# Optimization experiments

Measured on AMD Instinct MI355X. Metric: run time of the kernel, lower is better.

Reference implementation:

```python
import jax, jax.numpy as jnp
import numpy as np

N_LAYER, N_HEAD, N_EMBD, BLOCK, B, T = 8, 8, 1024, 1024, 2, 1024
LN_EPS = 1e-5


def _ln(x, w, b):
    m = jnp.mean(x, axis=-1, keepdims=True)
    v = jnp.mean(jnp.square(x - m), axis=-1, keepdims=True)
    return (x - m) * jax.lax.rsqrt(v + LN_EPS) * w + b


def setup_inputs() -> dict:
    key = jax.random.key(0)
    ks = jax.random.split(key, 8)
    L, C = N_LAYER, N_EMBD
    rn = lambda k, shape, s=0.02: jax.random.normal(k, shape, jnp.float32) * s
    return {
        "x": jax.random.normal(ks[0], (B, T, C), jnp.float32),
        "wpe": rn(ks[1], (BLOCK, C)),
        "ln1_w": jnp.ones((L, C), jnp.float32),
        "ln1_b": jnp.zeros((L, C), jnp.float32),
        "attn_w": rn(ks[2], (L, 3 * C, C)),
        "attn_b": jnp.zeros((L, 3 * C), jnp.float32),
        "proj_w": rn(ks[3], (L, C, C), 0.02 / np.sqrt(2 * L)),
        "proj_b": jnp.zeros((L, C), jnp.float32),
        "ln2_w": jnp.ones((L, C), jnp.float32),
        "ln2_b": jnp.zeros((L, C), jnp.float32),
        "fc_w": rn(ks[4], (L, 4 * C, C)),
        "fc_b": jnp.zeros((L, 4 * C), jnp.float32),
        "fcp_w": rn(ks[5], (L, C, 4 * C), 0.02 / np.sqrt(2 * L)),
        "fcp_b": jnp.zeros((L, C), jnp.float32),
        "lnf_w": jnp.ones((C,), jnp.float32),
        "lnf_b": jnp.zeros((C,), jnp.float32),
    }


def reference(x, wpe, ln1_w, ln1_b, attn_w, attn_b, proj_w, proj_b,
              ln2_w, ln2_b, fc_w, fc_b, fcp_w, fcp_b, lnf_w, lnf_b):
    Bb, Tt, C = x.shape
    H = N_HEAD
    D = C // H
    scale = jnp.float32(1.0 / np.sqrt(D))
    h = x + wpe[:Tt][None]  # pos emb broadcast over batch; dropout = identity (eval)
    causal = jnp.tril(jnp.ones((Tt, Tt), bool))  # [T,T]

    def block(h, p):
        l1w, l1b, aw, ab, pw, pb, l2w, l2b, fw, fb, pw2, pb2 = p
        xn = _ln(h, l1w, l1b)
        qkv = xn @ aw.T + ab  # [B,T,3C]
        q, k, v = jnp.split(qkv, 3, axis=-1)
        q = q.reshape(Bb, Tt, H, D).transpose(0, 2, 1, 3)  # bhtd
        k = k.reshape(Bb, Tt, H, D).transpose(0, 2, 1, 3)
        v = v.reshape(Bb, Tt, H, D).transpose(0, 2, 1, 3)
        att = jnp.einsum('bhtd,bhsd->bhts', q, k) * scale
        att = jnp.where(causal, att, -jnp.inf)
        att = jax.nn.softmax(att, axis=-1)
        y = jnp.einsum('bhts,bhsd->bhtd', att, v)
        y = y.transpose(0, 2, 1, 3).reshape(Bb, Tt, C)
        h = h + (y @ pw.T + pb)
        xn2 = _ln(h, l2w, l2b)
        m = jax.nn.gelu(xn2 @ fw.T + fb, approximate=True)  # matches NewGELU tanh form
        h = h + (m @ pw2.T + pb2)
        return h, None

    h, _ = jax.lax.scan(block, h, (ln1_w, ln1_b, attn_w, attn_b, proj_w, proj_b,
                                   ln2_w, ln2_b, fc_w, fc_b, fcp_w, fcp_b))
    return _ln(h, lnf_w, lnf_b)
```

## Files before the change

### kernel.cpp

```cpp
#include <hip/hip_runtime.h>

typedef unsigned short u16;
typedef __attribute__((ext_vector_type(8))) short short8;
typedef __attribute__((ext_vector_type(4))) float floatx4;

__device__ __forceinline__ u16 f2b(float f){
  unsigned u = __builtin_bit_cast(unsigned, f);
  u += 0x7FFFu + ((u >> 16) & 1u);
  return (u16)(u >> 16);
}

__device__ __forceinline__ float gelu_f(float x){
  float u = 0.7978845608028654f * (x + 0.044715f * x * x * x);
  float e = __expf(2.0f * u);
  return 0.5f * x * (2.0f - 2.0f / (e + 1.0f));
}

typedef const __attribute__((address_space(1))) unsigned int gas_u32;
typedef __attribute__((address_space(3))) unsigned int las_u32;
__device__ __forceinline__ void gll16(const void* g, void* l){
  __builtin_amdgcn_global_load_lds((gas_u32*)g, (las_u32*)l, 16, 0, 0);
}

__global__ __launch_bounds__(256) void k_cvt(const float* __restrict__ src,
                                             u16* __restrict__ dst){
  size_t e = ((size_t)blockIdx.x * 256 + threadIdx.x) * 4;
  float4 v = *(const float4*)(src + e);
  ushort4 o; o.x = f2b(v.x); o.y = f2b(v.y); o.z = f2b(v.z); o.w = f2b(v.w);
  *(ushort4*)(dst + e) = o;
}

__global__ __launch_bounds__(256) void k_addpos(const float* __restrict__ x,
                                                const float* __restrict__ wpe,
                                                float* __restrict__ h){
  size_t e = ((size_t)blockIdx.x * 256 + threadIdx.x) * 4;
  float4 a = *(const float4*)(x + e);
  float4 p = *(const float4*)(wpe + (e & 1048575u));
  float4 o; o.x = a.x + p.x; o.y = a.y + p.y; o.z = a.z + p.z; o.w = a.w + p.w;
  *(float4*)(h + e) = o;
}

__global__ __launch_bounds__(256) void k_layernorm(const float* __restrict__ x,
                                                   const float* __restrict__ w,
                                                   const float* __restrict__ b,
                                                   void* __restrict__ out, int out_bf16){
  int row = blockIdx.x, t = threadIdx.x;
  const float* xr = x + (size_t)row * 1024;
  float4 v = ((const float4*)xr)[t];
  float s1 = v.x + v.y + v.z + v.w;
  float s2 = v.x*v.x + v.y*v.y + v.z*v.z + v.w*v.w;
  #pragma unroll
  for (int off = 32; off > 0; off >>= 1){
    s1 += __shfl_down(s1, off);
    s2 += __shfl_down(s2, off);
  }
  __shared__ float p1[4], p2[4];
  if ((t & 63) == 0){ p1[t >> 6] = s1; p2[t >> 6] = s2; }
  __syncthreads();
  float S1 = p1[0] + p1[1] + p1[2] + p1[3];
  float S2 = p2[0] + p2[1] + p2[2] + p2[3];
  float mean = S1 * (1.0f / 1024.0f);
  float var  = S2 * (1.0f / 1024.0f) - mean * mean;
  float rs = rsqrtf(var + 1e-5f);
  float4 wv = ((const float4*)w)[t];
  float4 bv = ((const float4*)b)[t];
  float o0 = (v.x - mean) * rs * wv.x + bv.x;
  float o1 = (v.y - mean) * rs * wv.y + bv.y;
  float o2 = (v.z - mean) * rs * wv.z + bv.z;
  float o3 = (v.w - mean) * rs * wv.w + bv.w;
  if (out_bf16){
    ushort4 o; o.x = f2b(o0); o.y = f2b(o1); o.z = f2b(o2); o.w = f2b(o3);
    ((ushort4*)((u16*)out + (size_t)row * 1024))[t] = o;
  } else {
    float4 o; o.x = o0; o.y = o1; o.z = o2; o.w = o3;
    ((float4*)((float*)out + (size_t)row * 1024))[t] = o;
  }
}

template<int MODE>
__global__ __launch_bounds__(256) void k_gemm(
    const u16* __restrict__ A, int lda, long long A_bs, long long A_hs,
    const u16* __restrict__ B, int ldb, long long B_bs, long long B_hs,
    const float* __restrict__ bias,
    void* __restrict__ Out, int ldo, long long O_bs, long long O_hs,
    int Kdim, float scale, int causal, int n_ntiles, int Ksplit)
{
  int bx = blockIdx.x, by = blockIdx.y, bz = blockIdx.z;
  int nt = bx % n_ntiles, sp = bx / n_ntiles;
  if (MODE == 3 && nt > by) return;
  int m0 = by * 128, n0 = nt * 128;
  int kend_eff = (causal == 1) ? (m0 + 128 < Kdim ? m0 + 128 : Kdim) : Kdim;
  int ks = sp * Ksplit;
  int ke = ks + Ksplit < kend_eff ? ks + Ksplit : kend_eff;
  if (ks >= ke) return;
  int zb = bz >> 3, zh = bz & 7;
  A += (size_t)zb * A_bs + (size_t)zh * A_hs;
  B += (size_t)zb * B_bs + (size_t)zh * B_hs;
  size_t o_off = (size_t)zb * O_bs + (size_t)zh * O_hs;

  __shared__ u16 As[128 * 32];
  __shared__ u16 Bs[128 * 32];
  int t = threadIdx.x;
  int lane = t & 63, wid = t >> 6;
  int wm = (wid >> 1) * 64, wn = (wid & 1) * 64;
  int quad = lane >> 4, tm = lane & 15;
  int ar = t >> 2, ac = (t & 3) * 8;
  const u16* Ab = A + (size_t)(m0 + ar) * lda + ac;
  const u16* Bb = B + (size_t)(n0 + ar) * ldb + ac;
  u16* AsP0 = &As[t * 8];           u16* AsP1 = &As[2048 + t * 8];
  u16* BsP0 = &Bs[t * 8];           u16* BsP1 = &Bs[2048 + t * 8];
  const size_t a64 = (size_t)64 * lda, b64 = (size_t)64 * ldb;

  floatx4 acc[4][4] = {};
  for (int k0 = ks; k0 < ke; k0 += 32){
    __syncthreads();
    gll16(Ab + k0,        AsP0);
    gll16(Ab + a64 + k0,  AsP1);
    gll16(Bb + k0,        BsP0);
    gll16(Bb + b64 + k0,  BsP1);
    __syncthreads();
    short8 af[4], bf[4];
    #pragma unroll
    for (int i = 0; i < 4; i++)
      af[i] = *(const short8*)&As[(wm + i * 16 + tm) * 32 + quad * 8];
    #pragma unroll
    for (int j = 0; j < 4; j++)
      bf[j] = *(const short8*)&Bs[(wn + j * 16 + tm) * 32 + quad * 8];
    #pragma unroll
    for (int i = 0; i < 4; i++)
      #pragma unroll
      for (int j = 0; j < 4; j++)
        acc[i][j] = __builtin_amdgcn_mfma_f32_16x16x32_bf16(af[i], bf[j], acc[i][j], 0, 0, 0);
  }
  #pragma unroll
  for (int j = 0; j < 4; j++){
    int col = n0 + wn + j * 16 + tm;
    float bc = 0.0f;
    if ((MODE == 0 || MODE == 1) && bias) bc = bias[col];
    if (MODE == 2 && sp == 0 && bias) bc = bias[col];
    #pragma unroll
    for (int i = 0; i < 4; i++){
      int row0 = m0 + wm + i * 16 + quad * 4;
      #pragma unroll
      for (int r = 0; r < 4; r++){
        float v = acc[i][j][r] + bc;
        size_t idx = o_off + (size_t)(row0 + r) * ldo + col;
        if (MODE == 0)      ((u16*)Out)[idx] = f2b(v);
        else if (MODE == 1) ((u16*)Out)[idx] = f2b(gelu_f(v));
        else if (MODE == 3) ((float*)Out)[idx] = v * scale;
        else                atomicAdd((float*)Out + idx, v);
      }
    }
  }
}

__global__ __launch_bounds__(256) void k_transpose_v(const u16* __restrict__ vsrc,
                                                     u16* __restrict__ vt){
  __shared__ u16 tile[64][66];
  int bh = blockIdx.z, b = bh >> 3, hh = bh & 7;
  int d0 = blockIdx.x * 64, s0 = blockIdx.y * 64;
  const u16* src = vsrc + (size_t)b * 3145728 + hh * 128;
  int t = threadIdx.x;
  {
    int sr = t >> 4, c4 = (t & 15) * 4;
    #pragma unroll
    for (int p = 0; p < 4; p++){
      int s = sr + p * 16;
      ushort4 v = *(const ushort4*)(src + (size_t)(s0 + s) * 3072 + d0 + c4);
      tile[s][c4 + 0] = v.x; tile[s][c4 + 1] = v.y;
      tile[s][c4 + 2] = v.z; tile[s][c4 + 3] = v.w;
    }
  }
  __syncthreads();
  {
    int dr = t >> 4, s4 = (t & 15) * 4;
    #pragma unroll
    for (int p = 0; p < 4; p++){
      int d = dr + p * 16;
      ushort4 o;
      o.x = tile[s4 + 0][d]; o.y = tile[s4 + 1][d];
      o.z = tile[s4 + 2][d]; o.w = tile[s4 + 3][d];
      *(ushort4*)(vt + (size_t)bh * 131072 + (size_t)(d0 + d) * 1024 + s0 + s4) = o;
    }
  }
}

__global__ __launch_bounds__(256) void k_softmax(float* __restrict__ S){
  int bh = blockIdx.x >> 10, i = blockIdx.x & 1023;
  float* row = S + ((size_t)bh << 20) + ((size_t)i << 10);
  int t = threadIdx.x, j0 = t * 4;
  float4 v;
  if (j0 <= i) v = ((const float4*)row)[t];
  else { v.x = 0.0f; v.y = 0.0f; v.z = 0.0f; v.w = 0.0f; }
  float mx = -3.0e38f;
  if (j0 + 0 <= i) mx = fmaxf(mx, v.x);
  if (j0 + 1 <= i) mx = fmaxf(mx, v.y);
  if (j0 + 2 <= i) mx = fmaxf(mx, v.z);
  if (j0 + 3 <= i) mx = fmaxf(mx, v.w);
  #pragma unroll
  for (int off = 32; off > 0; off >>= 1) mx = fmaxf(mx, __shfl_down(mx, off));
  __shared__ float pm[4], ps[4];
  if ((t & 63) == 0) pm[t >> 6] = mx;
  __syncthreads();
  mx = fmaxf(fmaxf(pm[0], pm[1]), fmaxf(pm[2], pm[3]));
  float e0 = (j0 + 0 <= i) ? __expf(v.x - mx) : 0.0f;
  float e1 = (j0 + 1 <= i) ? __expf(v.y - mx) : 0.0f;
  float e2 = (j0 + 2 <= i) ? __expf(v.z - mx) : 0.0f;
  float e3 = (j0 + 3 <= i) ? __expf(v.w - mx) : 0.0f;
  float s = e0 + e1 + e2 + e3;
  #pragma unroll
  for (int off = 32; off > 0; off >>= 1) s += __shfl_down(s, off);
  if ((t & 63) == 0) ps[t >> 6] = s;
  __syncthreads();
  s = ps[0] + ps[1] + ps[2] + ps[3];
  float inv = 1.0f / s;
  ushort4 o; o.x = f2b(e0 * inv); o.y = f2b(e1 * inv);
  o.z = f2b(e2 * inv); o.w = f2b(e3 * inv);
  ((ushort4*)row)[t] = o;
}

extern "C" void kernel_launch(void* const* d_in, const int* in_sizes, int n_in,
                              void* d_out, int out_size, void* d_ws, size_t ws_size,
                              hipStream_t stream){
  const float* x     = (const float*)d_in[0];
  const float* wpe   = (const float*)d_in[1];
  const float* ln1w  = (const float*)d_in[2];
  const float* ln1b  = (const float*)d_in[3];
  const float* attnw = (const float*)d_in[4];
  const float* attnb = (const float*)d_in[5];
  const float* projw = (const float*)d_in[6];
  const float* projb = (const float*)d_in[7];
  const float* ln2w  = (const float*)d_in[8];
  const float* ln2b  = (const float*)d_in[9];
  const float* fcw   = (const float*)d_in[10];
  const float* fcb   = (const float*)d_in[11];
  const float* fcpw  = (const float*)d_in[12];
  const float* fcpb  = (const float*)d_in[13];
  const float* lnfw  = (const float*)d_in[14];
  const float* lnfb  = (const float*)d_in[15];

  char* ws = (char*)d_ws;
  float* h   = (float*)(ws);
  u16*   xn  = (u16*)(ws + 8388608);
  u16*   qkv = (u16*)(ws + 12582912);
  u16*   vt  = (u16*)(ws + 25165824);
  float* S   = (float*)(ws + 29360128);
  u16*   yb  = (u16*)(ws + 29360128);
  u16*   mlp = (u16*)(ws + 33554432);
  float* ybf = (float*)(ws + 96468992);
  u16*   wb  = (u16*)(ws + 104857600);

  k_addpos<<<2048, 256, 0, stream>>>(x, wpe, h);
  for (int l = 0; l < 8; l++){
    k_layernorm<<<2048, 256, 0, stream>>>(h, ln1w + l * 1024, ln1b + l * 1024, xn, 1);
    k_cvt<<<3072, 256, 0, stream>>>(attnw + (size_t)l * 3145728, wb);
    k_gemm<0><<<dim3(24, 16, 1), 256, 0, stream>>>(
        xn, 1024, 0, 0, wb, 1024, 0, 0, attnb + l * 3072,
        qkv, 3072, 0, 0, 1024, 1.0f, 0, 24, 1024);
    k_transpose_v<<<dim3(2, 16, 16), 256, 0, stream>>>(qkv + 2048, vt);
    k_gemm<3><<<dim3(8, 8, 16), 256, 0, stream>>>(
        qkv, 3072, 3145728LL, 128LL, qkv + 1024, 3072, 3145728LL, 128LL,
        nullptr, S, 1024, 8388608LL, 1048576LL, 128, 0.08838834764831845f, 2, 8, 128);
    k_softmax<<<16384, 256, 0, stream>>>(S);
    hipMemsetAsync(ybf, 0, 8388608, stream);
    k_gemm<4><<<dim3(4, 8, 16), 256, 0, stream>>>(
        (const u16*)S, 2048, 16777216LL, 2097152LL, vt, 1024, 1048576LL, 131072LL,
        nullptr, ybf, 1024, 1048576LL, 128LL, 1024, 1.0f, 1, 1, 256);
    k_cvt<<<2048, 256, 0, stream>>>(ybf, yb);
    k_cvt<<<1024, 256, 0, stream>>>(projw + (size_t)l * 1048576, wb);
    k_gemm<2><<<dim3(32, 16, 1), 256, 0, stream>>>(
        yb, 1024, 0, 0, wb, 1024, 0, 0, projb + l * 1024,
        h, 1024, 0, 0, 1024, 1.0f, 0, 8, 256);
    k_layernorm<<<2048, 256, 0, stream>>>(h, ln2w + l * 1024, ln2b + l * 1024, xn, 1);
    k_cvt<<<4096, 256, 0, stream>>>(fcw + (size_t)l * 4194304, wb);
    k_gemm<1><<<dim3(32, 16, 1), 256, 0, stream>>>(
        xn, 1024, 0, 0, wb, 1024, 0, 0, fcb + l * 4096,
        mlp, 4096, 0, 0, 1024, 1.0f, 0, 32, 1024);
    k_cvt<<<4096, 256, 0, stream>>>(fcpw + (size_t)l * 4194304, wb);
    k_gemm<2><<<dim3(32, 16, 1), 256, 0, stream>>>(
        mlp, 4096, 0, 0, wb, 4096, 0, 0, fcpb + l * 1024,
        h, 1024, 0, 0, 4096, 1.0f, 0, 8, 1024);
  }
  k_layernorm<<<2048, 256, 0, stream>>>(h, lnfw, lnfb, (float*)d_out, 0);
  (void)in_sizes; (void)n_in; (void)out_size; (void)ws_size;
}
```

Measured before the change: 2.240 ms.

## Fuse attention into flash kernel and pre-convert all layer weights once

Replaces the materialized score GEMM, separate softmax, split-K PV GEMM with atomics, memset and fp32-to-bf16 conversion with a single flash-attention kernel. It uses online softmax and a causal loop over 64-key tiles, writing bf16 outputs directly. This removes the large fp32 score matrix round trips through memory and several launches per layer. Weight conversion to bf16 is also hoisted out of the layer loop into four upfront launches, which needs more workspace. The flash kernel launches only 256 blocks with causally imbalanced work, so it may underutilize the GPU.

```diff
diff --git a/kernel.cpp b/kernel.cpp
--- a/kernel.cpp
+++ b/kernel.cpp
@@ -79,24 +79,18 @@
 
 template<int MODE>
 __global__ __launch_bounds__(256) void k_gemm(
-    const u16* __restrict__ A, int lda, long long A_bs, long long A_hs,
-    const u16* __restrict__ B, int ldb, long long B_bs, long long B_hs,
+    const u16* __restrict__ A, int lda,
+    const u16* __restrict__ B, int ldb,
     const float* __restrict__ bias,
-    void* __restrict__ Out, int ldo, long long O_bs, long long O_hs,
-    int Kdim, float scale, int causal, int n_ntiles, int Ksplit)
+    void* __restrict__ Out, int ldo,
+    int Kdim, int n_ntiles, int Ksplit)
 {
-  int bx = blockIdx.x, by = blockIdx.y, bz = blockIdx.z;
+  int bx = blockIdx.x, by = blockIdx.y;
   int nt = bx % n_ntiles, sp = bx / n_ntiles;
-  if (MODE == 3 && nt > by) return;
   int m0 = by * 128, n0 = nt * 128;
-  int kend_eff = (causal == 1) ? (m0 + 128 < Kdim ? m0 + 128 : Kdim) : Kdim;
   int ks = sp * Ksplit;
-  int ke = ks + Ksplit < kend_eff ? ks + Ksplit : kend_eff;
+  int ke = ks + Ksplit < Kdim ? ks + Ksplit : Kdim;
   if (ks >= ke) return;
-  int zb = bz >> 3, zh = bz & 7;
-  A += (size_t)zb * A_bs + (size_t)zh * A_hs;
-  B += (size_t)zb * B_bs + (size_t)zh * B_hs;
-  size_t o_off = (size_t)zb * O_bs + (size_t)zh * O_hs;
 
   __shared__ u16 As[128 * 32];
   __shared__ u16 Bs[128 * 32];
@@ -144,10 +138,9 @@
       #pragma unroll
       for (int r = 0; r < 4; r++){
         float v = acc[i][j][r] + bc;
-        size_t idx = o_off + (size_t)(row0 + r) * ldo + col;
+        size_t idx = (size_t)(row0 + r) * ldo + col;
         if (MODE == 0)      ((u16*)Out)[idx] = f2b(v);
         else if (MODE == 1) ((u16*)Out)[idx] = f2b(gelu_f(v));
-        else if (MODE == 3) ((float*)Out)[idx] = v * scale;
         else                atomicAdd((float*)Out + idx, v);
       }
     }
@@ -185,38 +178,115 @@
   }
 }
 
-__global__ __launch_bounds__(256) void k_softmax(float* __restrict__ S){
-  int bh = blockIdx.x >> 10, i = blockIdx.x & 1023;
-  float* row = S + ((size_t)bh << 20) + ((size_t)i << 10);
-  int t = threadIdx.x, j0 = t * 4;
-  float4 v;
-  if (j0 <= i) v = ((const float4*)row)[t];
-  else { v.x = 0.0f; v.y = 0.0f; v.z = 0.0f; v.w = 0.0f; }
-  float mx = -3.0e38f;
-  if (j0 + 0 <= i) mx = fmaxf(mx, v.x);
-  if (j0 + 1 <= i) mx = fmaxf(mx, v.y);
-  if (j0 + 2 <= i) mx = fmaxf(mx, v.z);
-  if (j0 + 3 <= i) mx = fmaxf(mx, v.w);
+__global__ __launch_bounds__(256) void k_flash(const u16* __restrict__ qkv,
+                                               const u16* __restrict__ vt,
+                                               u16* __restrict__ yb){
+  int qi = blockIdx.x, bh = blockIdx.y;
+  int b = bh >> 3, hh = bh & 7;
+  int t = threadIdx.x, lane = t & 63, w = t >> 6;
+  int quad = lane >> 4, tm = lane & 15;
+  const int q0 = qi * 64;
+  const u16* Qg  = qkv + (size_t)b * 3145728 + hh * 128;
+  const u16* Kg  = Qg + 1024;
+  const u16* Vtg = vt + (size_t)bh * 131072;
+  __shared__ u16 Ks[64 * 128];
+  __shared__ u16 Vs[128 * 64];
+  __shared__ u16 Ps[4][16 * 64];
+
+  short8 qf[4];
+  {
+    const u16* qr = Qg + (size_t)(q0 + w * 16 + tm) * 3072 + quad * 8;
+    #pragma unroll
+    for (int kk = 0; kk < 4; kk++) qf[kk] = *(const short8*)(qr + kk * 32);
+  }
+  floatx4 o_acc[8] = {};
+  float m_r[4], l_r[4];
   #pragma unroll
-  for (int off = 32; off > 0; off >>= 1) mx = fmaxf(mx, __shfl_down(mx, off));
-  __shared__ float pm[4], ps[4];
-  if ((t & 63) == 0) pm[t >> 6] = mx;
-  __syncthreads();
-  mx = fmaxf(fmaxf(pm[0], pm[1]), fmaxf(pm[2], pm[3]));
-  float e0 = (j0 + 0 <= i) ? __expf(v.x - mx) : 0.0f;
-  float e1 = (j0 + 1 <= i) ? __expf(v.y - mx) : 0.0f;
-  float e2 = (j0 + 2 <= i) ? __expf(v.z - mx) : 0.0f;
-  float e3 = (j0 + 3 <= i) ? __expf(v.w - mx) : 0.0f;
-  float s = e0 + e1 + e2 + e3;
+  for (int r = 0; r < 4; r++){ m_r[r] = -3.0e38f; l_r[r] = 0.0f; }
+  const float scale = 0.08838834764831845f;
+
+  for (int s0 = 0; s0 <= q0; s0 += 64){
+    __syncthreads();
+    {
+      int idx = w * 256 + lane;
+      #pragma unroll
+      for (int p = 0; p < 4; p++){
+        int id = idx + p * 64;
+        gll16(Kg + (size_t)(s0 + (id >> 4)) * 3072 + (id & 15) * 8, &Ks[id * 8]);
+      }
+      #pragma unroll
+      for (int p = 0; p < 4; p++){
+        int id = idx + p * 64;
+        gll16(Vtg + (size_t)(id >> 3) * 1024 + s0 + (id & 7) * 8, &Vs[id * 8]);
+      }
+    }
+    __syncthreads();
+    floatx4 s_acc[4] = {};
+    #pragma unroll
+    for (int j = 0; j < 4; j++)
+      #pragma unroll
+      for (int kk = 0; kk < 4; kk++){
+        short8 kf = *(const short8*)&Ks[(j * 16 + tm) * 128 + kk * 32 + quad * 8];
+        s_acc[j] = __builtin_amdgcn_mfma_f32_16x16x32_bf16(qf[kk], kf, s_acc[j], 0, 0, 0);
+      }
+    bool diag = (s0 == q0);
+    float sv[4][4];
+    #pragma unroll
+    for (int j = 0; j < 4; j++)
+      #pragma unroll
+      for (int r = 0; r < 4; r++){
+        float v = s_acc[j][r] * scale;
+        if (diag && (j * 16 + tm > w * 16 + quad * 4 + r)) v = -3.0e38f;
+        sv[j][r] = v;
+      }
+    float pv[4][4];
+    #pragma unroll
+    for (int r = 0; r < 4; r++){
+      float m = fmaxf(fmaxf(sv[0][r], sv[1][r]), fmaxf(sv[2][r], sv[3][r]));
+      #pragma unroll
+      for (int off = 8; off > 0; off >>= 1) m = fmaxf(m, __shfl_xor(m, off));
+      float m_new = fmaxf(m_r[r], m);
+      float alpha = __expf(m_r[r] - m_new);
+      m_r[r] = m_new;
+      float s = 0.0f;
+      #pragma unroll
+      for (int j = 0; j < 4; j++){
+        float p = __expf(sv[j][r] - m_new);
+        pv[j][r] = p; s += p;
+      }
+      #pragma unroll
+      for (int off = 8; off > 0; off >>= 1) s += __shfl_xor(s, off);
+      l_r[r] = l_r[r] * alpha + s;
+      #pragma unroll
+      for (int jd = 0; jd < 8; jd++) o_acc[jd][r] *= alpha;
+    }
+    u16* Pw = Ps[w];
+    #pragma unroll
+    for (int j = 0; j < 4; j++)
+      #pragma unroll
+      for (int r = 0; r < 4; r++)
+        Pw[(quad * 4 + r) * 64 + j * 16 + tm] = f2b(pv[j][r]);
+    __syncthreads();
+    short8 pf[2];
+    #pragma unroll
+    for (int kk = 0; kk < 2; kk++)
+      pf[kk] = *(const short8*)&Pw[tm * 64 + kk * 32 + quad * 8];
+    #pragma unroll
+    for (int jd = 0; jd < 8; jd++)
+      #pragma unroll
+      for (int kk = 0; kk < 2; kk++){
+        short8 vf = *(const short8*)&Vs[(jd * 16 + tm) * 64 + kk * 32 + quad * 8];
+        o_acc[jd] = __builtin_amdgcn_mfma_f32_16x16x32_bf16(pf[kk], vf, o_acc[jd], 0, 0, 0);
+      }
+  }
+  u16* yr = yb + ((size_t)b * 1024 + q0 + w * 16 + quad * 4) * 1024 + hh * 128;
   #pragma unroll
-  for (int off = 32; off > 0; off >>= 1) s += __shfl_down(s, off);
-  if ((t & 63) == 0) ps[t >> 6] = s;
-  __syncthreads();
-  s = ps[0] + ps[1] + ps[2] + ps[3];
-  float inv = 1.0f / s;
-  ushort4 o; o.x = f2b(e0 * inv); o.y = f2b(e1 * inv);
-  o.z = f2b(e2 * inv); o.w = f2b(e3 * inv);
-  ((ushort4*)row)[t] = o;
+  for (int r = 0; r < 4; r++){
+    float inv = 1.0f / l_r[r];
+    #pragma unroll
+    for (int jd = 0; jd < 8; jd++)
+      yr[(size_t)r * 1024 + jd * 16 + tm] = f2b(o_acc[jd][r] * inv);
+  }
 }
 
 extern "C" void kernel_launch(void* const* d_in, const int* in_sizes, int n_in,
@@ -240,46 +310,40 @@
   const float* lnfb  = (const float*)d_in[15];
 
   char* ws = (char*)d_ws;
-  float* h   = (float*)(ws);
-  u16*   xn  = (u16*)(ws + 8388608);
-  u16*   qkv = (u16*)(ws + 12582912);
-  u16*   vt  = (u16*)(ws + 25165824);
-  float* S   = (float*)(ws + 29360128);
-  u16*   yb  = (u16*)(ws + 29360128);
-  u16*   mlp = (u16*)(ws + 33554432);
-  float* ybf = (float*)(ws + 96468992);
-  u16*   wb  = (u16*)(ws + 104857600);
-
+  float* h    = (float*)(ws);
+  u16*   xn   = (u16*)(ws + 8388608);
+  u16*   qkv  = (u16*)(ws + 12582912);
+  u16*   vt   = (u16*)(ws + 25165824);
+  u16*   yb   = (u16*)(ws + 29360128);
+  u16*   mlp  = (u16*)(ws + 33554432);
+  u16*   wqkv = (u16*)(ws + 50331648);
+  u16*   wprj = (u16*)(ws + 100663296);
+  u16*   wfc  = (u16*)(ws + 117440512);
+  u16*   wfcp = (u16*)(ws + 184549376);
+
+  k_cvt<<<24576, 256, 0, stream>>>(attnw, wqkv);
+  k_cvt<<<8192,  256, 0, stream>>>(projw, wprj);
+  k_cvt<<<32768, 256, 0, stream>>>(fcw,  wfc);
+  k_cvt<<<32768, 256, 0, stream>>>(fcpw, wfcp);
   k_addpos<<<2048, 256, 0, stream>>>(x, wpe, h);
+
   for (int l = 0; l < 8; l++){
     k_layernorm<<<2048, 256, 0, stream>>>(h, ln1w + l * 1024, ln1b + l * 1024, xn, 1);
-    k_cvt<<<3072, 256, 0, stream>>>(attnw + (size_t)l * 3145728, wb);
-    k_gemm<0><<<dim3(24, 16, 1), 256, 0, stream>>>(
-        xn, 1024, 0, 0, wb, 1024, 0, 0, attnb + l * 3072,
-        qkv, 3072, 0, 0, 1024, 1.0f, 0, 24, 1024);
+    k_gemm<0><<<dim3(24, 16), 256, 0, stream>>>(
+        xn, 1024, wqkv + (size_t)l * 3145728, 1024, attnb + l * 3072,
+        qkv, 3072, 1024, 24, 1024);
     k_transpose_v<<<dim3(2, 16, 16), 256, 0, stream>>>(qkv + 2048, vt);
-    k_gemm<3><<<dim3(8, 8, 16), 256, 0, stream>>>(
-        qkv, 3072, 3145728LL, 128LL, qkv + 1024, 3072, 3145728LL, 128LL,
-        nullptr, S, 1024, 8388608LL, 1048576LL, 128, 0.08838834764831845f, 2, 8, 128);
-    k_softmax<<<16384, 256, 0, stream>>>(S);
-    hipMemsetAsync(ybf, 0, 8388608, stream);
-    k_gemm<4><<<dim3(4, 8, 16), 256, 0, stream>>>(
-        (const u16*)S, 2048, 16777216LL, 2097152LL, vt, 1024, 1048576LL, 131072LL,
-        nullptr, ybf, 1024, 1048576LL, 128LL, 1024, 1.0f, 1, 1, 256);
-    k_cvt<<<2048, 256, 0, stream>>>(ybf, yb);
-    k_cvt<<<1024, 256, 0, stream>>>(projw + (size_t)l * 1048576, wb);
-    k_gemm<2><<<dim3(32, 16, 1), 256, 0, stream>>>(
-        yb, 1024, 0, 0, wb, 1024, 0, 0, projb + l * 1024,
-        h, 1024, 0, 0, 1024, 1.0f, 0, 8, 256);
+    k_flash<<<dim3(16, 16), 256, 0, stream>>>(qkv, vt, yb);
+    k_gemm<2><<<dim3(32, 16), 256, 0, stream>>>(
+        yb, 1024, wprj + (size_t)l * 1048576, 1024, projb + l * 1024,
+        h, 1024, 1024, 8, 256);
     k_layernorm<<<2048, 256, 0, stream>>>(h, ln2w + l * 1024, ln2b + l * 1024, xn, 1);
-    k_cvt<<<4096, 256, 0, stream>>>(fcw + (size_t)l * 4194304, wb);
-    k_gemm<1><<<dim3(32, 16, 1), 256, 0, stream>>>(
-        xn, 1024, 0, 0, wb, 1024, 0, 0, fcb + l * 4096,
-        mlp, 4096, 0, 0, 1024, 1.0f, 0, 32, 1024);
-    k_cvt<<<4096, 256, 0, stream>>>(fcpw + (size_t)l * 4194304, wb);
-    k_gemm<2><<<dim3(32, 16, 1), 256, 0, stream>>>(
-        mlp, 4096, 0, 0, wb, 4096, 0, 0, fcpb + l * 1024,
-        h, 1024, 0, 0, 4096, 1.0f, 0, 8, 1024);
+    k_gemm<1><<<dim3(32, 16), 256, 0, stream>>>(
+        xn, 1024, wfc + (size_t)l * 4194304, 1024, fcb + l * 4096,
+        mlp, 4096, 1024, 32, 1024);
+    k_gemm<2><<<dim3(32, 16), 256, 0, stream>>>(
+        mlp, 4096, wfcp + (size_t)l * 4194304, 4096, fcpb + l * 1024,
+        h, 1024, 4096, 8, 1024);
   }
   k_layernorm<<<2048, 256, 0, stream>>>(h, lnfw, lnfb, (float*)d_out, 0);
   (void)in_sizes; (void)n_in; (void)out_size; (void)ws_size;
```

New measurement: 2.133 ms. 4.8% less time.
